# Performance work log

Measured on AMD Instinct MI355X. Metric: run time of the kernel, lower is better.

## Reference

```python
import jax, jax.numpy as jnp
import numpy as np

B, T, C, H = 2, 2048, 1024, 16  # batch, seq (== block_size), n_embd, n_head
HD = C // H  # head dim


def setup_inputs() -> dict:
    key = jax.random.key(0)
    k1, k2, k3 = jax.random.split(key, 3)
    x = jax.random.normal(k1, (B, T, C), dtype=jnp.float32)
    w_attn = jax.random.normal(k2, (C, 3 * C), dtype=jnp.float32) * (1.0 / np.sqrt(C))
    b_attn = jnp.zeros((3 * C,), dtype=jnp.float32)
    w_proj = jax.random.normal(k3, (C, C), dtype=jnp.float32) * (1.0 / np.sqrt(C))
    b_proj = jnp.zeros((C,), dtype=jnp.float32)
    return {"x": x, "w_attn": w_attn, "b_attn": b_attn, "w_proj": w_proj, "b_proj": b_proj}


def reference(x, w_attn, b_attn, w_proj, b_proj):
    # qkv projection: [B,T,3C]
    qkv = x @ w_attn + b_attn
    q, k, v = jnp.split(qkv, 3, axis=-1)
    # -> [B,H,T,HD]
    def to_heads(t):
        return t.reshape(B, T, H, HD).transpose(0, 2, 1, 3)
    q, k, v = to_heads(q), to_heads(k), to_heads(v)
    scale = 1.0 / np.sqrt(HD).astype(np.float32)
    # att: [B,H,T,T]
    att = jnp.einsum("bhqd,bhkd->bhqk", q, k) * scale
    causal = jnp.tril(jnp.ones((T, T), dtype=bool))
    att = jnp.where(causal[None, None], att, -jnp.inf)
    att = jax.nn.softmax(att, axis=-1)
    # y: [B,H,T,HD] -> [B,T,C]
    y = jnp.einsum("bhqk,bhkd->bhqd", att, v)
    y = y.transpose(0, 2, 1, 3).reshape(B, T, C)
    return y @ w_proj + b_proj
```

## Files before the change

kernel.cpp:

```cpp
#include <hip/hip_runtime.h>
#include <stdint.h>

#define Bb 2
#define Tt 2048
#define Cc 1024
#define Hh 16
#define HD 64
#define C3 3072

typedef __bf16 bf16x8 __attribute__((ext_vector_type(8)));
typedef float  f32x4  __attribute__((ext_vector_type(4)));
typedef unsigned short u16;
typedef u16 u16x8 __attribute__((ext_vector_type(8)));
typedef u16 u16x4 __attribute__((ext_vector_type(4)));

#define SCALE2 0.18033688f

__device__ __forceinline__ u16 f2bf(float f) {
  union { float f; unsigned u; } v; v.f = f;
  return (u16)((v.u + 0x7fffu + ((v.u >> 16) & 1u)) >> 16);
}
__device__ __forceinline__ float bf2f(u16 a) {
  union { unsigned u; float f; } v; v.u = ((unsigned)a) << 16; return v.f;
}

__device__ __forceinline__ void gl2lds16(const void* g, void* s) {
  __builtin_amdgcn_global_load_lds(
      (__attribute__((address_space(1))) void*)(g),
      (__attribute__((address_space(3))) void*)(s), 16, 0, 0);
}

__device__ __forceinline__ bf16x8 ldb8(const u16* p) {
  return __builtin_bit_cast(bf16x8, *(const u16x8*)p);
}

template <int N>
__device__ __forceinline__ void vmwait() {
  asm volatile("s_waitcnt vmcnt(%0)" :: "n"(N) : "memory");
}
__device__ __forceinline__ void barrier_nodrain() {
  __builtin_amdgcn_s_barrier();
  __builtin_amdgcn_sched_barrier(0);
}

__global__ __launch_bounds__(256)
void prep_kernel(const float* __restrict__ x, const float* __restrict__ w_attn,
                 const float* __restrict__ w_proj, u16* __restrict__ xb,
                 u16* __restrict__ wat, u16* __restrict__ wpt) {
  __shared__ u16 tile[64][65];
  const int blk = blockIdx.x;
  const int tid = threadIdx.x;
  if (blk < 4096) {
    int i = blk * 256 + tid;
    float4 v = ((const float4*)x)[i];
    u16x4 o = { f2bf(v.x), f2bf(v.y), f2bf(v.z), f2bf(v.w) };
    ((u16x4*)xb)[i] = o;
    return;
  }
  const float* in; u16* out; int R, C, c0, r0;
  if (blk < 4096 + 768) {
    int t = blk - 4096;
    in = w_attn; out = wat; R = 1024; C = 3072;
    c0 = (t % 48) * 64; r0 = (t / 48) * 64;
  } else {
    int t = blk - 4864;
    in = w_proj; out = wpt; R = 1024; C = 1024;
    c0 = (t & 15) * 64; r0 = (t >> 4) * 64;
  }
  int xx = tid & 63, yy = tid >> 6;
  #pragma unroll
  for (int rr = yy; rr < 64; rr += 4)
    tile[rr][xx] = f2bf(in[(size_t)(r0 + rr) * C + c0 + xx]);
  __syncthreads();
  #pragma unroll
  for (int rr = yy; rr < 64; rr += 4)
    out[(size_t)(c0 + rr) * R + r0 + xx] = tile[xx][rr];
}

template <int MODE, int BN, int MINW>
__global__ __launch_bounds__(256, MINW)
void gemm_bt(const u16* __restrict__ A, const u16* __restrict__ Bt,
             const float* __restrict__ bias, void* __restrict__ Cout,
             u16* __restrict__ Vt, int M, int N, int K) {
  __shared__ u16 As[3][128 * 32];
  __shared__ u16 Bs[3][BN * 32];
  constexpr int JT = BN / 32;
  constexpr int NB = BN / 128 + 1;
  constexpr int L  = 2 + NB;
  const int tid = threadIdx.x;
  const int ln  = tid & 63;
  const int w   = tid >> 6;
  const int wm  = w >> 1, wn = w & 1;
  const int l15 = ln & 15, lq = ln >> 4;
  const int swz2 = (l15 >> 1) & 3;
  const int m0 = blockIdx.y * 128, n0 = blockIdx.x * BN;

  int aoff[2], boff[NB];
  #pragma unroll
  for (int i = 0; i < 2; ++i) {
    int s = i * 256 + tid;
    int row = s >> 2, cg = (s & 3) ^ ((s >> 3) & 3);
    aoff[i] = (m0 + row) * K + cg * 8;
  }
  #pragma unroll
  for (int i = 0; i < NB; ++i) {
    int s = i * 256 + tid;
    int row = s >> 2, cg = (s & 3) ^ ((s >> 3) & 3);
    boff[i] = (n0 + row) * K + cg * 8;
  }

  f32x4 acc[4][JT];
  #pragma unroll
  for (int i = 0; i < 4; ++i)
    #pragma unroll
    for (int j = 0; j < JT; ++j)
      acc[i][j] = (f32x4){0.f, 0.f, 0.f, 0.f};

  const int NK = K >> 5;

  auto STAGE = [&](int buf, int t) {
    const int k0 = t * 32;
    #pragma unroll
    for (int i = 0; i < 2; ++i)
      gl2lds16(A + aoff[i] + k0, (char*)As[buf] + (size_t)(i * 256 + w * 64) * 16);
    #pragma unroll
    for (int i = 0; i < NB; ++i)
      gl2lds16(Bt + boff[i] + k0, (char*)Bs[buf] + (size_t)(i * 256 + w * 64) * 16);
  };

  STAGE(0, 0);
  if (NK > 1) STAGE(1, 1);

  int cur = 0;
  for (int it = 0; it < NK; ++it) {
    if (it + 1 < NK) vmwait<L>(); else vmwait<0>();
    barrier_nodrain();
    if (it + 2 < NK) STAGE(cur == 0 ? 2 : cur - 1, it + 2);
    const u16* AsB = As[cur];
    const u16* BsB = Bs[cur];
    bf16x8 af[4], bfr[JT];
    #pragma unroll
    for (int i = 0; i < 4; ++i)
      af[i] = ldb8(&AsB[(wm * 64 + i * 16 + l15) * 32 + ((lq ^ swz2) * 8)]);
    #pragma unroll
    for (int j = 0; j < JT; ++j)
      bfr[j] = ldb8(&BsB[(wn * (BN / 2) + j * 16 + l15) * 32 + ((lq ^ swz2) * 8)]);
    #pragma unroll
    for (int i = 0; i < 4; ++i)
      #pragma unroll
      for (int j = 0; j < JT; ++j)
        acc[i][j] = __builtin_amdgcn_mfma_f32_16x16x32_bf16(af[i], bfr[j], acc[i][j], 0, 0, 0);
    cur = (cur == 2) ? 0 : cur + 1;
  }

  if (MODE == 1 && n0 >= 2048) {
    #pragma unroll
    for (int i = 0; i < 4; ++i) {
      int rowb = m0 + wm * 64 + i * 16 + lq * 4;
      int b_ = rowb >> 11, t0 = rowb & 2047;
      int tl = t0 & 63;
      int c = tl >> 4, ll = (tl >> 2) & 3;
      int pos0 = (c >> 1) * 32 + ll * 8 + (c & 1) * 4;
      size_t tdst = (size_t)(t0 & ~63) + pos0;
      #pragma unroll
      for (int j = 0; j < JT; ++j) {
        int col = n0 + wn * (BN / 2) + j * 16 + l15;
        int hd = col - 2048;
        float bsv = bias[col];
        u16x4 pk;
        #pragma unroll
        for (int r = 0; r < 4; ++r) pk[r] = f2bf(acc[i][j][r] + bsv);
        *(u16x4*)&Vt[(size_t)(b_ * 1024 + hd) * Tt + tdst] = pk;
      }
    }
  } else {
    const int ldc = (MODE == 1) ? 2048 : N;
    #pragma unroll
    for (int i = 0; i < 4; ++i) {
      int row = m0 + wm * 64 + i * 16 + lq * 4;
      #pragma unroll
      for (int j = 0; j < JT; ++j) {
        int col = n0 + wn * (BN / 2) + j * 16 + l15;
        float bsv = bias[col];
        #pragma unroll
        for (int r = 0; r < 4; ++r) {
          float v = acc[i][j][r] + bsv;
          if (MODE == 1) ((u16*)Cout)[(size_t)(row + r) * ldc + col] = f2bf(v);
          else           ((float*)Cout)[(size_t)(row + r) * ldc + col] = v;
        }
      }
    }
  }
}


__device__ __forceinline__ bf16x8 packp(const f32x4& a, const f32x4& b) {
  bf16x8 r;
  #pragma unroll
  for (int i = 0; i < 4; ++i) { r[i] = (__bf16)a[i]; r[i + 4] = (__bf16)b[i]; }
  return r;
}
__device__ __forceinline__ bf16x8 qscale(const u16* p) {
  u16x8 q = *(const u16x8*)p;
  u16x8 s;
  #pragma unroll
  for (int j = 0; j < 8; ++j) s[j] = f2bf(bf2f(q[j]) * SCALE2);
  return __builtin_bit_cast(bf16x8, s);
}

__global__ __launch_bounds__(256, 2)
void attn_fused(const u16* __restrict__ qk, const u16* __restrict__ vt,
                u16* __restrict__ y) {
  __shared__ u16 Ks[2][128 * 64];
  __shared__ u16 Vts[2][64 * 128];
  const int tid = threadIdx.x;
  const int ln = tid & 63, w = tid >> 6;
  const int l15 = ln & 15, lq = ln >> 4;
  const int swzK = l15 & 7;
  const int bx = blockIdx.x;
  const int bh = bx & 31;
  const int h  = bh & 15, b = bh >> 4;
  const int rr_ = bx >> 8, g = (bx >> 5) & 7;
  const int qt = (rr_ == 0) ? 31 - g : (rr_ == 1) ? 16 + g : (rr_ == 2) ? 15 - g : g;
  const int q0w = qt * 64 + w * 16;

  const u16* qbase = qk + (size_t)(b * Tt) * 2048 + h * HD;
  const u16* kbase = qk + (size_t)(b * Tt) * 2048 + 1024 + h * HD;
  const u16* vbase = vt + (size_t)(b * 1024 + h * HD) * Tt;

  int koff[4], voff[4];
  #pragma unroll
  for (int i = 0; i < 4; ++i) {
    int s = i * 256 + tid;
    koff[i] = (s >> 3) * 2048 + (((s & 7) ^ ((s >> 3) & 7)) * 8);
    voff[i] = (s >> 4) * Tt + (((s & 15) ^ ((s >> 4) & 15)) * 8);
  }

  const u16* qrA = qbase + (size_t)(q0w + l15) * 2048;
  bf16x8 qA0 = qscale(qrA + lq * 8), qA1 = qscale(qrA + 32 + lq * 8);

  bf16x8 ones;
  #pragma unroll
  for (int j = 0; j < 8; ++j) ones[j] = (__bf16)1.0f;

  f32x4 o[4];
  #pragma unroll
  for (int j = 0; j < 4; ++j) o[j] = (f32x4){0, 0, 0, 0};
  f32x4 lacc = (f32x4){0, 0, 0, 0};
  float m = -__builtin_inff();
  const int qg = q0w + l15;
  const int nkv = (qt >> 1) + 1;

  auto STAGE = [&](int buf, int t) {
    const u16* ks = kbase + (size_t)(t * 128) * 2048;
    const u16* vs = vbase + t * 128;
    #pragma unroll
    for (int i = 0; i < 4; ++i) {
      gl2lds16(ks + koff[i], (char*)Ks[buf] + (size_t)(i * 256 + w * 64) * 16);
      gl2lds16(vs + voff[i], (char*)Vts[buf] + (size_t)(i * 256 + w * 64) * 16);
    }
  };

  STAGE(0, 0);
  int cur = 0;
  for (int it = 0; it < nkv; ++it) {
    const int kk = it * 128;
    __syncthreads();
    if (it + 1 < nkv) STAGE(cur ^ 1, it + 1);
    const u16* KsB  = Ks[cur];
    const u16* VtsB = Vts[cur];

    f32x4 t[8];
    #pragma unroll
    for (int i = 0; i < 8; ++i) t[i] = (f32x4){0, 0, 0, 0};
    __builtin_amdgcn_s_setprio(1);
    #pragma unroll
    for (int i = 0; i < 8; ++i) {
      bf16x8 kf0 = ldb8(&KsB[(i * 16 + l15) * 64 + ((lq      ^ swzK) * 8)]);
      bf16x8 kf1 = ldb8(&KsB[(i * 16 + l15) * 64 + (((lq + 4) ^ swzK) * 8)]);
      t[i] = __builtin_amdgcn_mfma_f32_16x16x32_bf16(kf0, qA0, t[i], 0, 0, 0);
      t[i] = __builtin_amdgcn_mfma_f32_16x16x32_bf16(kf1, qA1, t[i], 0, 0, 0);
    }
    __builtin_amdgcn_s_setprio(0);

    if (it == nkv - 1) {
      #pragma unroll
      for (int i = 0; i < 8; ++i)
        #pragma unroll
        for (int r = 0; r < 4; ++r) {
          int kv = kk + i * 16 + lq * 4 + r;
          if (kv > qg) t[i][r] = -__builtin_inff();
        }
    }

    float a0 = fmaxf(fmaxf(t[0][0], t[0][1]), fmaxf(t[0][2], t[0][3]));
    float a1 = fmaxf(fmaxf(t[1][0], t[1][1]), fmaxf(t[1][2], t[1][3]));
    float a2 = fmaxf(fmaxf(t[2][0], t[2][1]), fmaxf(t[2][2], t[2][3]));
    float a3 = fmaxf(fmaxf(t[3][0], t[3][1]), fmaxf(t[3][2], t[3][3]));
    float a4 = fmaxf(fmaxf(t[4][0], t[4][1]), fmaxf(t[4][2], t[4][3]));
    float a5 = fmaxf(fmaxf(t[5][0], t[5][1]), fmaxf(t[5][2], t[5][3]));
    float a6 = fmaxf(fmaxf(t[6][0], t[6][1]), fmaxf(t[6][2], t[6][3]));
    float a7 = fmaxf(fmaxf(t[7][0], t[7][1]), fmaxf(t[7][2], t[7][3]));
    float mx = fmaxf(fmaxf(fmaxf(a0, a1), fmaxf(a2, a3)),
                     fmaxf(fmaxf(a4, a5), fmaxf(a6, a7)));
    mx = fmaxf(mx, __shfl_xor(mx, 16));
#if __has_builtin(__builtin_amdgcn_permlane32_swap)
    {
      unsigned mu = __builtin_bit_cast(unsigned, mx);
      auto r2 = __builtin_amdgcn_permlane32_swap(mu, mu, false, false);
      mx = fmaxf(__builtin_bit_cast(float, (unsigned)r2[0]),
                 __builtin_bit_cast(float, (unsigned)r2[1]));
    }
#else
    mx = fmaxf(mx, __shfl_xor(mx, 32));
#endif

    if (!__all(mx <= m + 8.0f)) {
      float mn = fmaxf(m, mx);
      float al = __builtin_amdgcn_exp2f(m - mn);
      m = mn;
      lacc[0] *= al;
      #pragma unroll
      for (int jd = 0; jd < 4; ++jd)
        #pragma unroll
        for (int r = 0; r < 4; ++r) o[jd][r] *= al;
    }
    #pragma unroll
    for (int i = 0; i < 8; ++i)
      #pragma unroll
      for (int r = 0; r < 4; ++r)
        t[i][r] = __builtin_amdgcn_exp2f(t[i][r] - m);

    bf16x8 pk_[4];
    #pragma unroll
    for (int ks = 0; ks < 4; ++ks) pk_[ks] = packp(t[2 * ks], t[2 * ks + 1]);

    __builtin_amdgcn_s_setprio(1);
    #pragma unroll
    for (int ks = 0; ks < 4; ++ks) {
      lacc = __builtin_amdgcn_mfma_f32_16x16x32_bf16(ones, pk_[ks], lacc, 0, 0, 0);
      #pragma unroll
      for (int jd = 0; jd < 4; ++jd) {
        int d = jd * 16 + l15;
        bf16x8 vf = ldb8(&VtsB[d * 128 + (((ks * 4 + lq) ^ l15) * 8)]);
        o[jd] = __builtin_amdgcn_mfma_f32_16x16x32_bf16(vf, pk_[ks], o[jd], 0, 0, 0);
      }
    }
    __builtin_amdgcn_s_setprio(0);
    cur ^= 1;
  }

  float inv = 1.f / lacc[0];
  const size_t ybase = (size_t)(b * Tt + q0w + l15) * Cc + h * HD;
  #pragma unroll
  for (int jd = 0; jd < 4; ++jd) {
    u16x4 pk;
    #pragma unroll
    for (int r = 0; r < 4; ++r) pk[r] = f2bf(o[jd][r] * inv);
    *(u16x4*)&y[ybase + jd * 16 + lq * 4] = pk;
  }
}

extern "C" void kernel_launch(void* const* d_in, const int* in_sizes, int n_in,
                              void* d_out, int out_size, void* d_ws, size_t ws_size,
                              hipStream_t stream) {
  const float* x      = (const float*)d_in[0];
  const float* w_attn = (const float*)d_in[1];
  const float* b_attn = (const float*)d_in[2];
  const float* w_proj = (const float*)d_in[3];
  const float* b_proj = (const float*)d_in[4];
  float* out = (float*)d_out;

  char* ws = (char*)d_ws;
  u16* xb  = (u16*)(ws + 0);
  u16* wat = (u16*)(ws + 8388608);
  u16* wpt = (u16*)(ws + 14680064);
  u16* qkb = (u16*)(ws + 16777216);
  u16* vtb = (u16*)(ws + 33554432);
  u16* yb  = (u16*)(ws + 41943040);

  prep_kernel<<<5120, 256, 0, stream>>>(x, w_attn, w_proj, xb, wat, wpt);
  gemm_bt<1, 128, 3><<<dim3(24, 32), 256, 0, stream>>>(xb, wat, b_attn, (void*)qkb, vtb, 4096, 3072, 1024);
  attn_fused<<<1024, 256, 0, stream>>>(qkb, vtb, yb);
  gemm_bt<0, 64, 4><<<dim3(16, 32), 256, 0, stream>>>(yb, wpt, b_proj, (void*)out, nullptr, 4096, 1024, 1024);
}
```

Before: 171.9 us.

## Replace QKV projection GEMM with 256x256-tile, 512-thread pipelined kernel

Adds a new gemm256 kernel for the QKV projection that uses 256x256 output tiles, 8 waves, 64-deep K steps with double-buffered direct global-to-LDS loads, and an XOR-swizzled LDS layout. Loads for the next-next stage are interleaved between four MFMA sub-blocks, and the MFMA sections run at raised wave priority. The aim is more operand reuse per LDS byte and better overlap of loads with math. The trade-off is a much smaller grid (192 blocks on a chip with many CUs) and a large per-thread register and LDS footprint, which risks poor occupancy and tail effects. The old V-transpose epilogue is removed from gemm_bt, since gemm_bt now only serves the output projection.

```diff
diff --git a/kernel.cpp b/kernel.cpp
--- a/kernel.cpp
+++ b/kernel.cpp
@@ -75,6 +75,169 @@
   #pragma unroll
   for (int rr = yy; rr < 64; rr += 4)
     out[(size_t)(c0 + rr) * R + r0 + xx] = tile[xx][rr];
+}
+
+__global__ __launch_bounds__(512, 2)
+void gemm256(const u16* __restrict__ A, const u16* __restrict__ Bt,
+             const float* __restrict__ bias, u16* __restrict__ Cq,
+             u16* __restrict__ Vt, int M, int N, int K) {
+  __shared__ u16 As[2][256 * 64];
+  __shared__ u16 Bs[2][256 * 64];
+  const int tid = threadIdx.x;
+  const int ln = tid & 63, w = tid >> 6;
+  const int wm = w >> 2, wn = w & 3;
+  const int l15 = ln & 15, lq = ln >> 4;
+  const int m0 = blockIdx.y * 256, n0 = blockIdx.x * 256;
+
+  const int lrow = ln >> 3, lchunk = ln & 7;
+  const int laneoff = lrow * K + ((lchunk ^ lrow) * 8);
+
+  f32x4 acc[8][4];
+  #pragma unroll
+  for (int i = 0; i < 8; ++i)
+    #pragma unroll
+    for (int j = 0; j < 4; ++j) acc[i][j] = (f32x4){0.f, 0.f, 0.f, 0.f};
+
+  const int NK = K >> 6;
+
+  auto STAGE_A = [&](int buf, int t, int mh) {
+    #pragma unroll
+    for (int i = 0; i < 2; ++i) {
+      int r0 = i * 128 + mh * 64 + w * 8;
+      gl2lds16(A + (size_t)(m0 + r0) * K + t * 64 + laneoff,
+               (char*)As[buf] + (size_t)r0 * 128);
+    }
+  };
+  auto STAGE_B = [&](int buf, int t, int nh) {
+    #pragma unroll
+    for (int i = 0; i < 2; ++i) {
+      int r0 = (i * 2 + (w >> 2)) * 64 + nh * 32 + (w & 3) * 8;
+      gl2lds16(Bt + (size_t)(n0 + r0) * K + t * 64 + laneoff,
+               (char*)Bs[buf] + (size_t)r0 * 128);
+    }
+  };
+  auto LDA = [&](const u16* base, int mh, int mfq, int kk) {
+    int row = wm * 128 + mh * 64 + mfq * 16 + l15;
+    return ldb8(&base[row * 64 + (((kk * 4 + lq) ^ (l15 & 7)) * 8)]);
+  };
+  auto LDB = [&](const u16* base, int nh, int nfq, int kk) {
+    int row = wn * 64 + nh * 32 + nfq * 16 + l15;
+    return ldb8(&base[row * 64 + (((kk * 4 + lq) ^ (l15 & 7)) * 8)]);
+  };
+
+  STAGE_A(0, 0, 0); STAGE_A(0, 0, 1); STAGE_B(0, 0, 0); STAGE_B(0, 0, 1);
+  if (NK > 1) { STAGE_A(1, 1, 0); STAGE_A(1, 1, 1); STAGE_B(1, 1, 0); STAGE_B(1, 1, 1); }
+
+  for (int u = 0; u < NK; ++u) {
+    const int buf = u & 1;
+    const u16* AsB = As[buf];
+    const u16* BsB = Bs[buf];
+    const bool st = (u + 2 < NK);
+
+    if (u + 1 < NK) vmwait<8>(); else vmwait<0>();
+    barrier_nodrain();
+    bf16x8 afr[4][2], bfr0[2][2], bfr1[2][2];
+    #pragma unroll
+    for (int mfq = 0; mfq < 4; ++mfq)
+      #pragma unroll
+      for (int kk = 0; kk < 2; ++kk) afr[mfq][kk] = LDA(AsB, 0, mfq, kk);
+    #pragma unroll
+    for (int nfq = 0; nfq < 2; ++nfq)
+      #pragma unroll
+      for (int kk = 0; kk < 2; ++kk) bfr0[nfq][kk] = LDB(BsB, 0, nfq, kk);
+    __builtin_amdgcn_s_setprio(1);
+    #pragma unroll
+    for (int mfq = 0; mfq < 4; ++mfq)
+      #pragma unroll
+      for (int nfq = 0; nfq < 2; ++nfq)
+        #pragma unroll
+        for (int kk = 0; kk < 2; ++kk)
+          acc[mfq][nfq] = __builtin_amdgcn_mfma_f32_16x16x32_bf16(
+              afr[mfq][kk], bfr0[nfq][kk], acc[mfq][nfq], 0, 0, 0);
+    __builtin_amdgcn_s_setprio(0);
+
+    barrier_nodrain();
+    if (st) STAGE_A(buf, u + 2, 0);
+    #pragma unroll
+    for (int nfq = 0; nfq < 2; ++nfq)
+      #pragma unroll
+      for (int kk = 0; kk < 2; ++kk) bfr1[nfq][kk] = LDB(BsB, 1, nfq, kk);
+    __builtin_amdgcn_s_setprio(1);
+    #pragma unroll
+    for (int mfq = 0; mfq < 4; ++mfq)
+      #pragma unroll
+      for (int nfq = 0; nfq < 2; ++nfq)
+        #pragma unroll
+        for (int kk = 0; kk < 2; ++kk)
+          acc[mfq][2 + nfq] = __builtin_amdgcn_mfma_f32_16x16x32_bf16(
+              afr[mfq][kk], bfr1[nfq][kk], acc[mfq][2 + nfq], 0, 0, 0);
+    __builtin_amdgcn_s_setprio(0);
+
+    barrier_nodrain();
+    if (st) STAGE_B(buf, u + 2, 0);
+    #pragma unroll
+    for (int mfq = 0; mfq < 4; ++mfq)
+      #pragma unroll
+      for (int kk = 0; kk < 2; ++kk) afr[mfq][kk] = LDA(AsB, 1, mfq, kk);
+    __builtin_amdgcn_s_setprio(1);
+    #pragma unroll
+    for (int mfq = 0; mfq < 4; ++mfq)
+      #pragma unroll
+      for (int nfq = 0; nfq < 2; ++nfq)
+        #pragma unroll
+        for (int kk = 0; kk < 2; ++kk)
+          acc[4 + mfq][nfq] = __builtin_amdgcn_mfma_f32_16x16x32_bf16(
+              afr[mfq][kk], bfr0[nfq][kk], acc[4 + mfq][nfq], 0, 0, 0);
+    __builtin_amdgcn_s_setprio(0);
+
+    barrier_nodrain();
+    if (st) { STAGE_A(buf, u + 2, 1); STAGE_B(buf, u + 2, 1); }
+    __builtin_amdgcn_s_setprio(1);
+    #pragma unroll
+    for (int mfq = 0; mfq < 4; ++mfq)
+      #pragma unroll
+      for (int nfq = 0; nfq < 2; ++nfq)
+        #pragma unroll
+        for (int kk = 0; kk < 2; ++kk)
+          acc[4 + mfq][2 + nfq] = __builtin_amdgcn_mfma_f32_16x16x32_bf16(
+              afr[mfq][kk], bfr1[nfq][kk], acc[4 + mfq][2 + nfq], 0, 0, 0);
+    __builtin_amdgcn_s_setprio(0);
+  }
+
+  if (n0 >= 2048) {
+    #pragma unroll
+    for (int mf = 0; mf < 8; ++mf) {
+      int rowb = m0 + wm * 128 + mf * 16 + lq * 4;
+      int b_ = rowb >> 11, t0 = rowb & 2047;
+      int tl = t0 & 63;
+      int c = tl >> 4, ll = (tl >> 2) & 3;
+      int pos0 = (c >> 1) * 32 + ll * 8 + (c & 1) * 4;
+      size_t tdst = (size_t)(t0 & ~63) + pos0;
+      #pragma unroll
+      for (int nf = 0; nf < 4; ++nf) {
+        int col = n0 + wn * 64 + nf * 16 + l15;
+        int hd = col - 2048;
+        float bsv = bias[col];
+        u16x4 pk;
+        #pragma unroll
+        for (int r = 0; r < 4; ++r) pk[r] = f2bf(acc[mf][nf][r] + bsv);
+        *(u16x4*)&Vt[(size_t)(b_ * 1024 + hd) * Tt + tdst] = pk;
+      }
+    }
+  } else {
+    #pragma unroll
+    for (int mf = 0; mf < 8; ++mf) {
+      int row = m0 + wm * 128 + mf * 16 + lq * 4;
+      #pragma unroll
+      for (int nf = 0; nf < 4; ++nf) {
+        int col = n0 + wn * 64 + nf * 16 + l15;
+        float bsv = bias[col];
+        #pragma unroll
+        for (int r = 0; r < 4; ++r)
+          Cq[(size_t)(row + r) * 2048 + col] = f2bf(acc[mf][nf][r] + bsv);
+      }
+    }
+  }
 }
 
 template <int MODE, int BN, int MINW>
@@ -153,46 +316,23 @@
     cur = (cur == 2) ? 0 : cur + 1;
   }
 
-  if (MODE == 1 && n0 >= 2048) {
-    #pragma unroll
-    for (int i = 0; i < 4; ++i) {
-      int rowb = m0 + wm * 64 + i * 16 + lq * 4;
-      int b_ = rowb >> 11, t0 = rowb & 2047;
-      int tl = t0 & 63;
-      int c = tl >> 4, ll = (tl >> 2) & 3;
-      int pos0 = (c >> 1) * 32 + ll * 8 + (c & 1) * 4;
-      size_t tdst = (size_t)(t0 & ~63) + pos0;
-      #pragma unroll
-      for (int j = 0; j < JT; ++j) {
-        int col = n0 + wn * (BN / 2) + j * 16 + l15;
-        int hd = col - 2048;
-        float bsv = bias[col];
-        u16x4 pk;
-        #pragma unroll
-        for (int r = 0; r < 4; ++r) pk[r] = f2bf(acc[i][j][r] + bsv);
-        *(u16x4*)&Vt[(size_t)(b_ * 1024 + hd) * Tt + tdst] = pk;
+  const int ldc = (MODE == 1) ? 2048 : N;
+  #pragma unroll
+  for (int i = 0; i < 4; ++i) {
+    int row = m0 + wm * 64 + i * 16 + lq * 4;
+    #pragma unroll
+    for (int j = 0; j < JT; ++j) {
+      int col = n0 + wn * (BN / 2) + j * 16 + l15;
+      float bsv = bias[col];
+      #pragma unroll
+      for (int r = 0; r < 4; ++r) {
+        float v = acc[i][j][r] + bsv;
+        if (MODE == 1) ((u16*)Cout)[(size_t)(row + r) * ldc + col] = f2bf(v);
+        else           ((float*)Cout)[(size_t)(row + r) * ldc + col] = v;
       }
     }
-  } else {
-    const int ldc = (MODE == 1) ? 2048 : N;
-    #pragma unroll
-    for (int i = 0; i < 4; ++i) {
-      int row = m0 + wm * 64 + i * 16 + lq * 4;
-      #pragma unroll
-      for (int j = 0; j < JT; ++j) {
-        int col = n0 + wn * (BN / 2) + j * 16 + l15;
-        float bsv = bias[col];
-        #pragma unroll
-        for (int r = 0; r < 4; ++r) {
-          float v = acc[i][j][r] + bsv;
-          if (MODE == 1) ((u16*)Cout)[(size_t)(row + r) * ldc + col] = f2bf(v);
-          else           ((float*)Cout)[(size_t)(row + r) * ldc + col] = v;
-        }
-      }
-    }
-  }
-}
-
+  }
+}
 
 __device__ __forceinline__ bf16x8 packp(const f32x4& a, const f32x4& b) {
   bf16x8 r;
@@ -380,7 +520,7 @@
   u16* yb  = (u16*)(ws + 41943040);
 
   prep_kernel<<<5120, 256, 0, stream>>>(x, w_attn, w_proj, xb, wat, wpt);
-  gemm_bt<1, 128, 3><<<dim3(24, 32), 256, 0, stream>>>(xb, wat, b_attn, (void*)qkb, vtb, 4096, 3072, 1024);
+  gemm256<<<dim3(12, 16), 512, 0, stream>>>(xb, wat, b_attn, qkb, vtb, 4096, 3072, 1024);
   attn_fused<<<1024, 256, 0, stream>>>(qkb, vtb, yb);
   gemm_bt<0, 64, 4><<<dim3(16, 32), 256, 0, stream>>>(yb, wpt, b_proj, (void*)out, nullptr, 4096, 1024, 1024);
 }
```

Result: slower. 179.7 us (+4.6%).
